# Kernel optimization log

Measured on AMD Instinct MI355X. Metric: run time of the kernel, lower is better.

Reference implementation:

```python
import jax, jax.numpy as jnp
import numpy as np

N = 300000
GRID = 256
K = 27  # 3x3x3 kernel offsets
C = 128


def _build_neighbors(rng):
    # sample unique occupied voxels in a GRID^3 lattice (sorted linear ids)
    lin = np.unique(rng.integers(0, GRID ** 3, size=int(N * 1.3)))[:N]
    z = lin // (GRID * GRID)
    y = (lin // GRID) % GRID
    x = lin % GRID
    nbr = np.full((N, K), -1, np.int32)
    k = 0
    for dz in (-1, 0, 1):
        for dy in (-1, 0, 1):
            for dx in (-1, 0, 1):
                nz, ny, nx = z + dz, y + dy, x + dx
                valid = (nz >= 0) & (nz < GRID) & (ny >= 0) & (ny < GRID) & (nx >= 0) & (nx < GRID)
                nlin = (nz * GRID + ny) * GRID + nx
                pos = np.clip(np.searchsorted(lin, nlin), 0, N - 1)
                found = valid & (lin[pos] == nlin)
                nbr[:, k] = np.where(found, pos, -1).astype(np.int32)
                k += 1
    return nbr


def setup_inputs() -> dict:
    key = jax.random.key(0)
    ks = jax.random.split(key, 8)
    s = 0.05
    rng = np.random.default_rng(0)
    nbr_idx = jnp.asarray(_build_neighbors(rng))
    return {
        "x_feat": jnp.ones((N, 1), jnp.float32),
        "W_in": jax.random.normal(ks[0], (K, 1, C), jnp.float32) * s,
        "b_in": jnp.zeros((C,), jnp.float32),
        "W_res": jax.random.normal(ks[1], (3, 2, K, C, C), jnp.float32) * s,
        "b_res": jnp.zeros((3, 2, C), jnp.float32),
        "W_out": jax.random.normal(ks[2], (K, C, C), jnp.float32) * s,
        "b_out": jnp.zeros((C,), jnp.float32),
        "Wf1": jax.random.normal(ks[3], (C, C), jnp.float32) * s,
        "bf1": jnp.zeros((C,), jnp.float32),
        "Wf2": jax.random.normal(ks[4], (C, C), jnp.float32) * s,
        "bf2": jnp.zeros((C,), jnp.float32),
        "Wf3": jax.random.normal(ks[5], (C, 3), jnp.float32) * s,
        "bf3": jnp.zeros((3,), jnp.float32),
        "nbr_idx": nbr_idx,
    }


def _sconv(x, nbr, W, b):
    # sparse 3^3 conv: per-offset gather -> GEMM -> masked accumulate
    # x: [N,Cin], nbr: [N,K] (-1 = no neighbor), W: [K,Cin,Cout]
    Cout = W.shape[-1]
    def body(k, acc):
        idx = nbr[:, k]
        g = jnp.where((idx >= 0)[:, None], x[jnp.maximum(idx, 0)], 0.0)
        return acc + g @ W[k]
    acc = jnp.zeros((x.shape[0], Cout), x.dtype)
    return jax.lax.fori_loop(0, W.shape[0], body, acc) + b


def _decoder(x_feat, nbr, W_in, b_in, W_res, b_res, W_out, b_out, Wf1, bf1, Wf2, bf2, Wf3, bf3):
    h = jax.nn.relu(_sconv(x_feat, nbr, W_in, b_in))
    for i in range(W_res.shape[0]):  # ResNetBlock: conv-relu-conv + residual
        r = jax.nn.relu(_sconv(h, nbr, W_res[i, 0], b_res[i, 0]))
        r = _sconv(r, nbr, W_res[i, 1], b_res[i, 1])
        h = h + r
    h = _sconv(h, nbr, W_out, b_out)
    # fc stack of 1x1 convs (pointwise GEMMs)
    h = jax.nn.relu(h @ Wf1 + bf1)
    h = jax.nn.relu(h @ Wf2 + bf2)
    return h @ Wf3 + bf3  # [N,3] predicted coordinate offsets


def reference(x_feat, W_in, b_in, W_res, b_res, W_out, b_out, Wf1, bf1, Wf2, bf2, Wf3, bf3, nbr_idx):
    return _decoder(x_feat, nbr_idx, W_in, b_in, W_res, b_res, W_out, b_out, Wf1, bf1, Wf2, bf2, Wf3, bf3)
```

## Files before the change

### kernel.cpp

```cpp
#include <hip/hip_runtime.h>
#include <hip/hip_bf16.h>
#include <stdint.h>

#define NNODES 300000
#define KNBR   27
#define CDIM   128
#define P_ROWS   219968
#define MAXTILES 2048
#define MAXSLOT  16
#define NT_SELF  ((NNODES + 127) / 128)
#define SELF_GRID 512


typedef __bf16 bf16x8_t __attribute__((ext_vector_type(8)));
typedef __bf16 bf16x4_t __attribute__((ext_vector_type(4)));
typedef float  f32x4_t  __attribute__((ext_vector_type(4)));

union BP8 { bf16x8_t v; __hip_bfloat16 h[8]; };
union BP4 { bf16x4_t v; __hip_bfloat16 h[4]; };

__device__ __forceinline__ void gl2lds16(const void* g, void* l) {
  __builtin_amdgcn_global_load_lds(
      reinterpret_cast<const __attribute__((address_space(1))) uint32_t*>(
          reinterpret_cast<uintptr_t>(g)),
      reinterpret_cast<__attribute__((address_space(3))) uint32_t*>(
          reinterpret_cast<uintptr_t>(l)),
      16, 0, 0);
}

__global__ void prep_weights(const float* __restrict__ Wres,
                             const float* __restrict__ Wout,
                             const float* __restrict__ Wf1,
                             const float* __restrict__ Wf2,
                             __hip_bfloat16* __restrict__ wbf) {
  int b = blockIdx.x;
  int m = b >> 7;
  int cout = b & 127;
  int cin = threadIdx.x;
  const float* src;
  if (m < 162)      src = Wres + (size_t)m * 16384;
  else if (m < 189) src = Wout + (size_t)(m - 162) * 16384;
  else if (m == 189) src = Wf1;
  else               src = Wf2;
  float v = src[cin * 128 + cout];
  int sp = (cin & 15) * 8 + (cin >> 4);
  wbf[(size_t)m * 16384 + cout * 128 + sp] = __float2bfloat16(v);
}

__global__ void prep_bias(const float* __restrict__ b_res,
                          const float* __restrict__ b_out,
                          const float* __restrict__ bf1,
                          const float* __restrict__ bf2,
                          float* __restrict__ bp) {
  int v = blockIdx.x;
  int p = threadIdx.x;
  const float* src;
  if (v < 6)       src = b_res + v * 128;
  else if (v == 6) src = b_out;
  else if (v == 7) src = bf1;
  else             src = bf2;
  bp[v * 128 + p] = src[(p & 7) * 16 + (p >> 3)];
}

__global__ void prep_win(const float* __restrict__ Win,
                         __hip_bfloat16* __restrict__ WinT) {
  int c = threadIdx.x;
  for (int k = 0; k < 32; ++k)
    WinT[c * 32 + k] = __float2bfloat16(k < 27 ? Win[k * 128 + c] : 0.0f);
}

__global__ void init_meta(int* __restrict__ segcnt, __hip_bfloat16* __restrict__ z) {
  int t = threadIdx.x;
  if (t < 32) segcnt[t] = 0;
  if (t == 0) { segcnt[128] = 0; segcnt[129] = 0; }
  z[t] = __float2bfloat16(0.0f);
}

__global__ void count_pairs(const int* __restrict__ nbr, int* __restrict__ segcnt,
                            unsigned int* __restrict__ nmask,
                            int* __restrict__ vlist) {
  __shared__ int lc[27];
  int t = threadIdx.x;
  if (t < 27) lc[t] = 0;
  __syncthreads();
  int n = blockIdx.x * 256 + t;
  if (n < NNODES) {
    int nb[27];
    #pragma unroll
    for (int k = 0; k < 27; ++k) nb[k] = nbr[n * 27 + k];
    unsigned int mask = 0;
    #pragma unroll
    for (int k = 0; k < 27; ++k)
      if (k != 13 && nb[k] >= 0) mask |= (1u << k);
    int pc = __popc(mask);
    while (pc > MAXSLOT) {
      mask &= ~(1u << (31 - __clz((int)mask)));
      --pc;
    }
    unsigned int m = mask;
    int j = 0;
    while (m) {
      int k = __ffs(m) - 1; m &= m - 1;
      vlist[n * MAXSLOT + j] = nb[k]; ++j;
      atomicAdd(&lc[k], 1);
    }
    nmask[n] = mask;
  }
  __syncthreads();
  if (t < 27 && t != 13 && lc[t]) atomicAdd(&segcnt[t], lc[t]);
}

__global__ void scan_tiles(const int* __restrict__ segcnt,
                           int* __restrict__ segbase, int* __restrict__ seglen,
                           int* __restrict__ cursor,
                           int* __restrict__ tile_k, int* __restrict__ tile_row0,
                           int* __restrict__ tile_rows,
                           int* __restrict__ ntile) {
  __shared__ int sbase[27], slen[27], tbase[27];
  int t = threadIdx.x;
  for (int i = t; i < MAXTILES; i += 256) tile_k[i] = -1;
  if (t < 32) cursor[t] = 0;
  if (t == 0) {
    int base = 0, tb = 0;
    for (int k = 0; k < 27; ++k) {
      int c = (k == 13) ? 0 : segcnt[k];
      if (base + c > P_ROWS) c = P_ROWS - base;
      if (c < 0) c = 0;
      sbase[k] = base; slen[k] = c; tbase[k] = tb;
      base += c;
      tb += (c + 127) >> 7;
    }
    ntile[0] = tb;
  }
  __syncthreads();
  if (t < 27) {
    segbase[t] = sbase[t];
    seglen[t] = slen[t];
    if (t != 13) {
      int idx = tbase[t];
      for (int r = 0; r < slen[t]; r += 128, ++idx) {
        if (idx < MAXTILES) {
          tile_k[idx] = t;
          tile_row0[idx] = sbase[t] + r;
          tile_rows[idx] = (slen[t] - r < 128) ? (slen[t] - r) : 128;
        }
      }
    }
  }
}

__global__ void fill_pairs(const unsigned int* __restrict__ nmask,
                           const int* __restrict__ vlist,
                           const int* __restrict__ segbase, const int* __restrict__ seglen,
                           int* __restrict__ cursor,
                           int* __restrict__ pr_src, int* __restrict__ pr_dst,
                           int* __restrict__ dinfo, int* __restrict__ dcursor) {
  __shared__ int lc[27], lb[27];
  __shared__ int dloc, dbase_s;
  int t = threadIdx.x;
  if (t < 27) lc[t] = 0;
  if (t == 0) dloc = 0;
  __syncthreads();
  int n = blockIdx.x * 256 + t;
  unsigned int mask = (n < NNODES) ? nmask[n] : 0u;
  int myj = __popc(mask);
  int myoff = myj ? atomicAdd(&dloc, myj) : 0;
  unsigned int m = mask;
  while (m) { int k = __ffs(m) - 1; m &= m - 1; atomicAdd(&lc[k], 1); }
  __syncthreads();
  if (t < 27) { lb[t] = lc[t] ? atomicAdd(&cursor[t], lc[t]) : 0; lc[t] = 0; }
  if (t == 0) dbase_s = dloc ? atomicAdd(dcursor, dloc) : 0;
  __syncthreads();
  if (n < NNODES) {
    int dbase = dbase_s + myoff;
    int jj = 0, vidx = 0;
    m = mask;
    while (m) {
      int k = __ffs(m) - 1; m &= m - 1;
      int lp = atomicAdd(&lc[k], 1);
      int pos = lb[k] + lp;
      if (pos < seglen[k]) {
        int slot = segbase[k] + pos;
        pr_src[slot] = vlist[n * MAXSLOT + vidx];
        pr_dst[slot] = dbase + jj;
        ++jj;
      }
      ++vidx;
    }
    dinfo[n] = (dbase << 5) | jj;
  }
}

__global__ void build_g(const float* __restrict__ xf, const int* __restrict__ nbr,
                        __hip_bfloat16* __restrict__ G) {
  int e = blockIdx.x * 256 + threadIdx.x;
  if (e >= NNODES * 32) return;
  int n = e >> 5, j = e & 31;
  float v = 0.0f;
  if (j < 27) {
    int idx = nbr[n * 27 + j];
    if (idx >= 0) v = xf[idx];
  }
  G[e] = __float2bfloat16(v);
}

__global__ __launch_bounds__(256, 2)
void l1_gemm(const __hip_bfloat16* __restrict__ G,
             const __hip_bfloat16* __restrict__ WinT,
             const float* __restrict__ bin,
             __hip_bfloat16* __restrict__ Aout) {
  __shared__ unsigned short As[128 * 32];

  const int t    = threadIdx.x;
  const int wid  = t >> 6;
  const int lane = t & 63;
  const int quad = lane >> 4;
  const int l16  = lane & 15;
  const int m0   = blockIdx.x * 128;
  const int m_base = (wid & 1) * 64;
  const int n_base = (wid >> 1) * 64;

  bf16x8_t bfr[4];
  #pragma unroll
  for (int ni = 0; ni < 4; ++ni)
    bfr[ni] = *(const bf16x8_t*)(WinT + (n_base + ni * 16 + l16) * 32 + quad * 8);

  float bv[4];
  #pragma unroll
  for (int ni = 0; ni < 4; ++ni) bv[ni] = bin[n_base + ni * 16 + l16];

  const char* Gb = (const char*)(G + (size_t)m0 * 32);
  #pragma unroll
  for (int i = 0; i < 2; ++i) {
    int row = i * 64 + (t >> 2);
    int slot = t & 3;
    gl2lds16(Gb + (size_t)row * 64 + ((slot ^ (row & 3)) * 16),
             (char*)As + i * 4096 + t * 16);
  }
  __syncthreads();

  f32x4_t acc[4][4];
  #pragma unroll
  for (int i = 0; i < 4; ++i)
    #pragma unroll
    for (int j = 0; j < 4; ++j)
      acc[i][j] = (f32x4_t){0.f, 0.f, 0.f, 0.f};

  bf16x8_t af[4];
  #pragma unroll
  for (int mi = 0; mi < 4; ++mi)
    af[mi] = *(const bf16x8_t*)(As + (m_base + mi * 16 + l16) * 32 +
                                ((quad ^ (l16 & 3)) * 8));
  #pragma unroll
  for (int mi = 0; mi < 4; ++mi)
    #pragma unroll
    for (int ni = 0; ni < 4; ++ni)
      acc[mi][ni] = __builtin_amdgcn_mfma_f32_16x16x32_bf16(af[mi], bfr[ni], acc[mi][ni], 0, 0, 0);

  const int nb4 = n_base >> 4;
  #pragma unroll
  for (int mi = 0; mi < 4; ++mi)
    #pragma unroll
    for (int r = 0; r < 4; ++r) {
      int node = m0 + m_base + mi * 16 + quad * 4 + r;
      if (node < NNODES) {
        BP4 o;
        #pragma unroll
        for (int ni = 0; ni < 4; ++ni) {
          float v = acc[mi][ni][r] + bv[ni];
          v = v > 0.0f ? v : 0.0f;
          o.h[ni] = __float2bfloat16(v);
        }
        *(bf16x4_t*)(Aout + (size_t)node * 128 + l16 * 8 + nb4) = o.v;
      }
    }
}

__global__ __launch_bounds__(256, 3)
void pair_gemm(const __hip_bfloat16* __restrict__ Ain,
               const __hip_bfloat16* __restrict__ Wl,
               const int* __restrict__ pr_src,
               const int* __restrict__ pr_dst,
               const int* __restrict__ tile_k, const int* __restrict__ tile_row0,
               const int* __restrict__ tile_rows,
               __hip_bfloat16* __restrict__ P,
               const __hip_bfloat16* __restrict__ zrow) {
  __shared__ unsigned short Ws[128 * 128];

  const int tk = tile_k[blockIdx.x];
  if (tk < 0) return;
  const int row0 = tile_row0[blockIdx.x];
  const int rows = tile_rows[blockIdx.x];

  const int t    = threadIdx.x;
  const int wid  = t >> 6;
  const int lane = t & 63;
  const int quad = lane >> 4;
  const int l16  = lane & 15;
  const int m_base = wid * 32;

  {
    const char* wsrc = (const char*)(Wl + (size_t)tk * 16384);
    #pragma unroll
    for (int i = 0; i < 8; ++i) {
      int row = wid * 32 + i * 4 + quad;
      gl2lds16(wsrc + (uint32_t)row * 256 + (uint32_t)((l16 ^ (row & 7)) * 16),
               (char*)Ws + wid * 8192 + i * 1024 + lane * 16);
    }
  }

  const __hip_bfloat16* rp[2];
  #pragma unroll
  for (int mi = 0; mi < 2; ++mi) {
    int row = m_base + mi * 16 + l16;
    rp[mi] = zrow;
    if (row < rows) rp[mi] = Ain + (size_t)pr_src[row0 + row] * 128;
  }
  int dst[2][4];
  #pragma unroll
  for (int mi = 0; mi < 2; ++mi)
    #pragma unroll
    for (int r = 0; r < 4; ++r) {
      int row = m_base + mi * 16 + quad * 4 + r;
      dst[mi][r] = (row < rows) ? pr_dst[row0 + row] : -1;
    }

  __syncthreads();

  f32x4_t acc[2][8];
  #pragma unroll
  for (int i = 0; i < 2; ++i)
    #pragma unroll
    for (int j = 0; j < 8; ++j)
      acc[i][j] = (f32x4_t){0.f, 0.f, 0.f, 0.f};

  #pragma unroll
  for (int kk = 0; kk < 4; ++kk) {
    bf16x8_t af[2];
    #pragma unroll
    for (int mi = 0; mi < 2; ++mi)
      af[mi] = *(const bf16x8_t*)(rp[mi] + kk * 32 + quad * 8);
    #pragma unroll
    for (int ni = 0; ni < 8; ++ni) {
      bf16x8_t bw = *(const bf16x8_t*)(Ws + (ni * 16 + l16) * 128 +
                                       (((kk * 4 + quad) ^ (l16 & 7)) * 8));
      #pragma unroll
      for (int mi = 0; mi < 2; ++mi)
        acc[mi][ni] = __builtin_amdgcn_mfma_f32_16x16x32_bf16(af[mi], bw, acc[mi][ni], 0, 0, 0);
    }
  }

  #pragma unroll
  for (int mi = 0; mi < 2; ++mi)
    #pragma unroll
    for (int r = 0; r < 4; ++r) {
      if (dst[mi][r] >= 0) {
        BP8 o;
        #pragma unroll
        for (int ni = 0; ni < 8; ++ni)
          o.h[ni] = __float2bfloat16(acc[mi][ni][r]);
        *(bf16x8_t*)(P + (size_t)dst[mi][r] * 128 + l16 * 8) = o.v;
      }
    }
}

template <int EPI, bool HASP>
__global__ __launch_bounds__(256, 2)
void self_gemm(const __hip_bfloat16* __restrict__ Ain,
               const __hip_bfloat16* __restrict__ W13,
               const float* __restrict__ bp,
               const __hip_bfloat16* __restrict__ P,
               const int* __restrict__ dinfo,
               __hip_bfloat16* __restrict__ Aout,
               const __hip_bfloat16* __restrict__ zrow) {
  const int t    = threadIdx.x;
  const int wid  = t >> 6;
  const int lane = t & 63;
  const int quad = lane >> 4;
  const int l16  = lane & 15;
  const int m_base = wid * 32;

  bf16x8_t bfr[8][4];
  #pragma unroll
  for (int ni = 0; ni < 8; ++ni)
    #pragma unroll
    for (int kk = 0; kk < 4; ++kk)
      bfr[ni][kk] = *(const bf16x8_t*)(W13 + (ni * 16 + l16) * 128 + kk * 32 + quad * 8);

  float bb[8];
  {
    f32x4_t b0 = *(const f32x4_t*)(bp + l16 * 8);
    f32x4_t b1 = *(const f32x4_t*)(bp + l16 * 8 + 4);
    #pragma unroll
    for (int i = 0; i < 4; ++i) { bb[i] = b0[i]; bb[i + 4] = b1[i]; }
  }

  #pragma unroll 1
  for (int tile = blockIdx.x; tile < NT_SELF; tile += gridDim.x) {
    const int m0 = tile * 128;

    int dif[2][4];
    if (HASP) {
      #pragma unroll
      for (int mi = 0; mi < 2; ++mi)
        #pragma unroll
        for (int r = 0; r < 4; ++r) {
          int node = m0 + m_base + mi * 16 + quad * 4 + r;
          dif[mi][r] = (node < NNODES) ? dinfo[node] : 0;
        }
    }

    f32x4_t acc[2][8];
    #pragma unroll
    for (int i = 0; i < 2; ++i)
      #pragma unroll
      for (int j = 0; j < 8; ++j)
        acc[i][j] = (f32x4_t){0.f, 0.f, 0.f, 0.f};

    const __hip_bfloat16* Abase = Ain + (size_t)(m0 + m_base + l16) * 128;

    #pragma unroll
    for (int kk = 0; kk < 4; ++kk) {
      bf16x8_t af[2];
      #pragma unroll
      for (int mi = 0; mi < 2; ++mi)
        af[mi] = *(const bf16x8_t*)(Abase + mi * 2048 + kk * 32 + quad * 8);
      #pragma unroll
      for (int mi = 0; mi < 2; ++mi)
        #pragma unroll
        for (int ni = 0; ni < 8; ++ni)
          acc[mi][ni] = __builtin_amdgcn_mfma_f32_16x16x32_bf16(af[mi], bfr[ni][kk], acc[mi][ni], 0, 0, 0);
    }

    #pragma unroll
    for (int mi = 0; mi < 2; ++mi) {
      const int nodeb = m0 + m_base + mi * 16 + quad * 4;
      bf16x8_t hold[4], pf[4];
      int cnt4[4], base4[4];
      #pragma unroll
      for (int r = 0; r < 4; ++r) {
        int node = nodeb + r;
        bool ok = node < NNODES;
        if (EPI == 1)
          hold[r] = *(const bf16x8_t*)((ok ? Aout + (size_t)node * 128 : zrow) + l16 * 8);
        if (HASP) {
          int d = dif[mi][r];
          cnt4[r] = d & 31;
          base4[r] = d >> 5;
          pf[r] = *(const bf16x8_t*)((cnt4[r] > 0 ? P + (size_t)base4[r] * 128 : zrow) + l16 * 8);
        }
      }
      #pragma unroll
      for (int r = 0; r < 4; ++r) {
        int node = nodeb + r;
        if (node >= NNODES) continue;
        float add[8];
        #pragma unroll
        for (int ni = 0; ni < 8; ++ni) add[ni] = bb[ni];
        if (HASP) {
          if (cnt4[r] > 0) {
            #pragma unroll
            for (int ni = 0; ni < 8; ++ni) add[ni] += (float)pf[r][ni];
          }
          for (int j = 1; j < cnt4[r]; ++j) {
            bf16x8_t pv = *(const bf16x8_t*)(P + (size_t)(base4[r] + j) * 128 + l16 * 8);
            #pragma unroll
            for (int ni = 0; ni < 8; ++ni) add[ni] += (float)pv[ni];
          }
        }
        BP8 o;
        #pragma unroll
        for (int ni = 0; ni < 8; ++ni) {
          float v = acc[mi][ni][r] + add[ni];
          if (EPI == 0) {
            v = v > 0.0f ? v : 0.0f;
            o.h[ni] = __float2bfloat16(v);
          } else if (EPI == 1) {
            o.h[ni] = __float2bfloat16((float)hold[r][ni] + v);
          } else {
            o.h[ni] = __float2bfloat16(v);
          }
        }
        *(bf16x8_t*)(Aout + (size_t)node * 128 + l16 * 8) = o.v;
      }
    }
  }
}

__global__ __launch_bounds__(256, 2)
void fc_fused(const __hip_bfloat16* __restrict__ Ain,
              const __hip_bfloat16* __restrict__ W1,
              const __hip_bfloat16* __restrict__ W2,
              const float* __restrict__ bp1,
              const float* __restrict__ bp2,
              const float* __restrict__ Wf3,
              const float* __restrict__ bf3,
              float* __restrict__ out) {
  __shared__ unsigned short S0[16384];
  __shared__ unsigned short S1[16384];

  const int t    = threadIdx.x;
  const int wid  = t >> 6;
  const int lane = t & 63;
  const int quad = lane >> 4;
  const int l16  = lane & 15;
  const int m_base = wid * 32;
  const int m0   = blockIdx.x * 128;

  #pragma unroll
  for (int i = 0; i < 8; ++i) {
    int row = wid * 32 + i * 4 + quad;
    uint32_t goff = (uint32_t)row * 256 + (uint32_t)((l16 ^ (row & 7)) * 16);
    gl2lds16((const char*)W1 + goff, (char*)S0 + wid * 8192 + i * 1024 + lane * 16);
    gl2lds16((const char*)W2 + goff, (char*)S1 + wid * 8192 + i * 1024 + lane * 16);
  }

  float bb1[8], bb2[8];
  {
    f32x4_t a0 = *(const f32x4_t*)(bp1 + l16 * 8);
    f32x4_t a1 = *(const f32x4_t*)(bp1 + l16 * 8 + 4);
    f32x4_t c0 = *(const f32x4_t*)(bp2 + l16 * 8);
    f32x4_t c1 = *(const f32x4_t*)(bp2 + l16 * 8 + 4);
    #pragma unroll
    for (int i = 0; i < 4; ++i) {
      bb1[i] = a0[i]; bb1[i + 4] = a1[i];
      bb2[i] = c0[i]; bb2[i + 4] = c1[i];
    }
  }
  float wf[8][3];
  #pragma unroll
  for (int ni = 0; ni < 8; ++ni)
    #pragma unroll
    for (int j = 0; j < 3; ++j)
      wf[ni][j] = Wf3[(ni * 16 + l16) * 3 + j];
  float b30 = bf3[0], b31 = bf3[1], b32 = bf3[2];

  __syncthreads();

  f32x4_t acc[2][8];
  #pragma unroll
  for (int i = 0; i < 2; ++i)
    #pragma unroll
    for (int j = 0; j < 8; ++j)
      acc[i][j] = (f32x4_t){0.f, 0.f, 0.f, 0.f};

  const __hip_bfloat16* Abase = Ain + (size_t)(m0 + m_base + l16) * 128;
  #pragma unroll
  for (int kk = 0; kk < 4; ++kk) {
    bf16x8_t af[2];
    #pragma unroll
    for (int mi = 0; mi < 2; ++mi)
      af[mi] = *(const bf16x8_t*)(Abase + mi * 2048 + kk * 32 + quad * 8);
    #pragma unroll
    for (int ni = 0; ni < 8; ++ni) {
      bf16x8_t bw = *(const bf16x8_t*)(S0 + (ni * 16 + l16) * 128 +
                                       (((kk * 4 + quad) ^ (l16 & 7)) * 8));
      #pragma unroll
      for (int mi = 0; mi < 2; ++mi)
        acc[mi][ni] = __builtin_amdgcn_mfma_f32_16x16x32_bf16(af[mi], bw, acc[mi][ni], 0, 0, 0);
    }
  }

  __syncthreads();

  #pragma unroll
  for (int mi = 0; mi < 2; ++mi)
    #pragma unroll
    for (int r = 0; r < 4; ++r) {
      int row = m_base + mi * 16 + quad * 4 + r;
      BP8 o;
      #pragma unroll
      for (int ni = 0; ni < 8; ++ni) {
        float v = acc[mi][ni][r] + bb1[ni];
        v = v > 0.0f ? v : 0.0f;
        o.h[ni] = __float2bfloat16(v);
      }
      *(bf16x8_t*)((char*)S0 + (uint32_t)row * 256 + ((l16 ^ (row & 7)) * 16)) = o.v;
    }
  __syncthreads();

  #pragma unroll
  for (int i = 0; i < 2; ++i)
    #pragma unroll
    for (int j = 0; j < 8; ++j)
      acc[i][j] = (f32x4_t){0.f, 0.f, 0.f, 0.f};

  #pragma unroll
  for (int kk = 0; kk < 4; ++kk) {
    bf16x8_t af[2];
    #pragma unroll
    for (int mi = 0; mi < 2; ++mi) {
      int row = m_base + mi * 16 + l16;
      af[mi] = *(const bf16x8_t*)((char*)S0 + (uint32_t)row * 256 +
                                  (((kk * 4 + quad) ^ (row & 7)) * 16));
    }
    #pragma unroll
    for (int ni = 0; ni < 8; ++ni) {
      bf16x8_t bw = *(const bf16x8_t*)(S1 + (ni * 16 + l16) * 128 +
                                       (((kk * 4 + quad) ^ (l16 & 7)) * 8));
      #pragma unroll
      for (int mi = 0; mi < 2; ++mi)
        acc[mi][ni] = __builtin_amdgcn_mfma_f32_16x16x32_bf16(af[mi], bw, acc[mi][ni], 0, 0, 0);
    }
  }

  #pragma unroll
  for (int mi = 0; mi < 2; ++mi)
    #pragma unroll
    for (int r = 0; r < 4; ++r) {
      int node = m0 + m_base + mi * 16 + quad * 4 + r;
      float a0 = 0.f, a1 = 0.f, a2 = 0.f;
      #pragma unroll
      for (int ni = 0; ni < 8; ++ni) {
        float v = acc[mi][ni][r] + bb2[ni];
        v = v > 0.0f ? v : 0.0f;
        v = (float)__float2bfloat16(v);
        a0 += v * wf[ni][0];
        a1 += v * wf[ni][1];
        a2 += v * wf[ni][2];
      }
      #pragma unroll
      for (int s = 8; s >= 1; s >>= 1) {
        a0 += __shfl_xor(a0, s);
        a1 += __shfl_xor(a1, s);
        a2 += __shfl_xor(a2, s);
      }
      if (l16 == 0 && node < NNODES) {
        out[node * 3 + 0] = a0 + b30;
        out[node * 3 + 1] = a1 + b31;
        out[node * 3 + 2] = a2 + b32;
      }
    }
}

__global__ void layer1_kernel(const float* __restrict__ xf,
                              const float* __restrict__ Win,
                              const float* __restrict__ bin,
                              const int* __restrict__ nbr,
                              __hip_bfloat16* __restrict__ abf) {
  int n = blockIdx.x;
  int c = threadIdx.x;
  float acc = bin[c];
  #pragma unroll 9
  for (int k = 0; k < KNBR; ++k) {
    int idx = nbr[n * KNBR + k];
    if (idx >= 0) acc += xf[idx] * Win[k * 128 + c];
  }
  acc = acc > 0.0f ? acc : 0.0f;
  int sp = (c & 15) * 8 + (c >> 4);
  abf[(size_t)n * 128 + sp] = __float2bfloat16(acc);
}

template <int EPI>
__global__ __launch_bounds__(256, 2)
void sconv_kernel(const __hip_bfloat16* __restrict__ Ain,
                  const __hip_bfloat16* __restrict__ Wt,
                  const float* __restrict__ bias,
                  const int* __restrict__ nbr,
                  int nk,
                  __hip_bfloat16* __restrict__ Aout,
                  const __hip_bfloat16* __restrict__ zrow) {
  __shared__ unsigned short As[128 * 128];
  __shared__ unsigned short Bs[128 * 128];

  const int t    = threadIdx.x;
  const int wid  = t >> 6;
  const int lane = t & 63;
  const int quad = lane >> 4;
  const int l16  = lane & 15;
  const int m0   = blockIdx.x * 128;

  f32x4_t acc[4][4];
  #pragma unroll
  for (int i = 0; i < 4; ++i)
    #pragma unroll
    for (int j = 0; j < 4; ++j)
      acc[i][j] = (f32x4_t){0.f, 0.f, 0.f, 0.f};

  const int m_base = (wid & 1) * 64;
  const int n_base = (wid >> 1) * 64;

  for (int k = 0; k < nk; ++k) {
    {
      const char* wsrc = (const char*)(Wt + (size_t)k * 16384);
      #pragma unroll
      for (int i = 0; i < 8; ++i) {
        uint32_t off = (uint32_t)wid * 8192 + (uint32_t)i * 1024;
        int row = wid * 32 + i * 4 + quad;
        uint32_t goff = (uint32_t)row * 256 + (uint32_t)((l16 ^ (row & 7)) * 16);
        gl2lds16(wsrc + goff, (char*)Bs + off);
      }
    }
    {
      #pragma unroll
      for (int i = 0; i < 8; ++i) {
        int r = i * 16 + wid * 4 + quad;
        int node = m0 + r;
        const __hip_bfloat16* rowp;
        if (nbr) {
          int idx = (node < NNODES) ? nbr[node * KNBR + k] : -1;
          rowp = (idx >= 0) ? (Ain + (size_t)idx * 128) : zrow;
        } else {
          rowp = (node < NNODES) ? (Ain + (size_t)node * 128) : zrow;
        }
        uint32_t ldsoff = (uint32_t)(i * 16 + wid * 4) * 256;
        gl2lds16((const char*)rowp + ((l16 ^ (r & 7)) * 16), (char*)As + ldsoff);
      }
    }
    __syncthreads();

    #pragma unroll
    for (int kk = 0; kk < 4; ++kk) {
      const int p = ((kk * 4 + quad) ^ (l16 & 7)) * 8;
      bf16x8_t af[4], bfr[4];
      #pragma unroll
      for (int mi = 0; mi < 4; ++mi)
        af[mi] = *(const bf16x8_t*)(As + (m_base + mi * 16 + l16) * 128 + p);
      #pragma unroll
      for (int ni = 0; ni < 4; ++ni)
        bfr[ni] = *(const bf16x8_t*)(Bs + (n_base + ni * 16 + l16) * 128 + p);
      #pragma unroll
      for (int mi = 0; mi < 4; ++mi)
        #pragma unroll
        for (int ni = 0; ni < 4; ++ni)
          acc[mi][ni] = __builtin_amdgcn_mfma_f32_16x16x32_bf16(af[mi], bfr[ni], acc[mi][ni], 0, 0, 0);
    }
    __syncthreads();
  }

  const int nb4 = n_base >> 4;
  #pragma unroll
  for (int ni = 0; ni < 4; ++ni) {
    int sp = l16 * 8 + nb4 + ni;
    float bvv = bias[sp];
    #pragma unroll
    for (int mi = 0; mi < 4; ++mi) {
      #pragma unroll
      for (int r = 0; r < 4; ++r) {
        int row = m_base + mi * 16 + quad * 4 + r;
        int node = m0 + row;
        if (node < NNODES) {
          float v = acc[mi][ni][r] + bvv;
          size_t o = (size_t)node * 128 + sp;
          if (EPI == 0) {
            v = v > 0.0f ? v : 0.0f;
            Aout[o] = __float2bfloat16(v);
          } else if (EPI == 1) {
            Aout[o] = __float2bfloat16(__bfloat162float(Aout[o]) + v);
          } else {
            Aout[o] = __float2bfloat16(v);
          }
        }
      }
    }
  }
}

__global__ void fc3_kernel(const __hip_bfloat16* __restrict__ r,
                           const float* __restrict__ W,
                           const float* __restrict__ b,
                           float* __restrict__ out) {
  int n = blockIdx.x * 256 + threadIdx.x;
  if (n >= NNODES) return;
  float a0 = b[0], a1 = b[1], a2 = b[2];
  const bf16x8_t* rp = (const bf16x8_t*)(r + (size_t)n * 128);
  #pragma unroll
  for (int c8 = 0; c8 < 16; ++c8) {
    bf16x8_t v8 = rp[c8];
    #pragma unroll
    for (int j = 0; j < 8; ++j) {
      float v = (float)v8[j];
      int c = j * 16 + c8;
      a0 += v * W[c * 3 + 0];
      a1 += v * W[c * 3 + 1];
      a2 += v * W[c * 3 + 2];
    }
  }
  out[n * 3 + 0] = a0;
  out[n * 3 + 1] = a1;
  out[n * 3 + 2] = a2;
}

extern "C" void kernel_launch(void* const* d_in, const int* in_sizes, int n_in,
                              void* d_out, int out_size, void* d_ws, size_t ws_size,
                              hipStream_t stream) {
  const float* x_feat = (const float*)d_in[0];
  const float* W_in   = (const float*)d_in[1];
  const float* b_in   = (const float*)d_in[2];
  const float* W_res  = (const float*)d_in[3];
  const float* b_res  = (const float*)d_in[4];
  const float* W_out  = (const float*)d_in[5];
  const float* b_out  = (const float*)d_in[6];
  const float* Wf1    = (const float*)d_in[7];
  const float* bf1    = (const float*)d_in[8];
  const float* Wf2    = (const float*)d_in[9];
  const float* bf2    = (const float*)d_in[10];
  const float* Wf3    = (const float*)d_in[11];
  const float* bf3    = (const float*)d_in[12];
  const int*   nbr    = (const int*)d_in[13];
  float* out = (float*)d_out;

  char* ws = (char*)d_ws;
  __hip_bfloat16* abf0 = (__hip_bfloat16*)ws;
  __hip_bfloat16* abf1 = (__hip_bfloat16*)(ws +  76800000);
  __hip_bfloat16* wbf  = (__hip_bfloat16*)(ws + 153600000);
  __hip_bfloat16* zrow = (__hip_bfloat16*)(ws + 159858688);
  __hip_bfloat16* P    = (__hip_bfloat16*)(ws + 159858944);
  __hip_bfloat16* WinT = (__hip_bfloat16*)(ws + 159858944 + 56320000 - 8192);
  int* pr_dst    = (int*)(ws + 216178944);
  unsigned int* nmask = (unsigned int*)(ws + 217058944);
  int* dinfo     = (int*)(ws + 235378944);
  int* pr_src    = (int*)(ws + 236578944);
  int* segcnt    = (int*)(ws + 237458944);
  int* segbase   = segcnt + 32;
  int* seglen    = segcnt + 64;
  int* cursor    = segcnt + 96;
  int* ntile     = segcnt + 128;
  int* dcursor   = segcnt + 129;
  int* tile_k    = (int*)(ws + 237463040);
  int* tile_row0 = tile_k + MAXTILES;
  int* tile_rows = tile_k + 2 * MAXTILES;
  float* bp      = (float*)(ws + 237487616);
  __hip_bfloat16* G = abf1;
  int* vlist = (int*)P;
  const size_t SPARSE_NEED = 237487616 + 4608 + 512;

  const int GB = (NNODES + 127) / 128;
  __hip_bfloat16* W0 = wbf;

  prep_weights<<<191 * 128, 128, 0, stream>>>(W_res, W_out, Wf1, Wf2, wbf);
  init_meta<<<1, 128, 0, stream>>>(segcnt, zrow);

  if (ws_size >= SPARSE_NEED) {
    prep_bias<<<9, 128, 0, stream>>>(b_res, b_out, bf1, bf2, bp);
    prep_win<<<1, 128, 0, stream>>>(W_in, WinT);
    build_g<<<(NNODES * 32 + 255) / 256, 256, 0, stream>>>(x_feat, nbr, G);
    l1_gemm<<<GB, 256, 0, stream>>>(G, WinT, b_in, abf0);

    const int CB2 = (NNODES + 255) / 256;
    count_pairs<<<CB2, 256, 0, stream>>>(nbr, segcnt, nmask, vlist);
    scan_tiles<<<1, 256, 0, stream>>>(segcnt, segbase, seglen, cursor,
                                      tile_k, tile_row0, tile_rows, ntile);
    fill_pairs<<<CB2, 256, 0, stream>>>(nmask, vlist, segbase, seglen, cursor,
                                        pr_src, pr_dst, dinfo, dcursor);

    #define CONV(IN, OUT, WLAYER, BV, EPI)                                             \
      pair_gemm<<<MAXTILES, 256, 0, stream>>>(IN, WLAYER, pr_src, pr_dst,              \
                                              tile_k, tile_row0, tile_rows,            \
                                              P, zrow);                                \
      self_gemm<EPI, true><<<SELF_GRID, 256, 0, stream>>>(IN, (WLAYER) + 13 * 16384,   \
                                                          bp + (BV) * 128, P, dinfo,   \
                                                          OUT, zrow);

    CONV(abf0, abf1, W0 +   0 * 16384, 0, 0)
    CONV(abf1, abf0, W0 +  27 * 16384, 1, 1)
    CONV(abf0, abf1, W0 +  54 * 16384, 2, 0)
    CONV(abf1, abf0, W0 +  81 * 16384, 3, 1)
    CONV(abf0, abf1, W0 + 108 * 16384, 4, 0)
    CONV(abf1, abf0, W0 + 135 * 16384, 5, 1)
    CONV(abf0, abf1, W0 + 162 * 16384, 6, 2)
    #undef CONV

    fc_fused<<<GB, 256, 0, stream>>>(abf1, W0 + 189 * 16384, W0 + 190 * 16384,
                                     bp + 7 * 128, bp + 8 * 128, Wf3, bf3, out);
  } else {
    prep_bias<<<9, 128, 0, stream>>>(b_res, b_out, bf1, bf2, bp);
    layer1_kernel<<<NNODES, 128, 0, stream>>>(x_feat, W_in, b_in, nbr, abf0);
    sconv_kernel<0><<<GB, 256, 0, stream>>>(abf0, W0 +   0 * 16384, bp + 0 * 128, nbr, 27, abf1, zrow);
    sconv_kernel<1><<<GB, 256, 0, stream>>>(abf1, W0 +  27 * 16384, bp + 1 * 128, nbr, 27, abf0, zrow);
    sconv_kernel<0><<<GB, 256, 0, stream>>>(abf0, W0 +  54 * 16384, bp + 2 * 128, nbr, 27, abf1, zrow);
    sconv_kernel<1><<<GB, 256, 0, stream>>>(abf1, W0 +  81 * 16384, bp + 3 * 128, nbr, 27, abf0, zrow);
    sconv_kernel<0><<<GB, 256, 0, stream>>>(abf0, W0 + 108 * 16384, bp + 4 * 128, nbr, 27, abf1, zrow);
    sconv_kernel<1><<<GB, 256, 0, stream>>>(abf1, W0 + 135 * 16384, bp + 5 * 128, nbr, 27, abf0, zrow);
    sconv_kernel<2><<<GB, 256, 0, stream>>>(abf0, W0 + 162 * 16384, bp + 6 * 128, nbr, 27, abf1, zrow);
    sconv_kernel<0><<<GB, 256, 0, stream>>>(abf1, W0 + 189 * 16384, bp + 7 * 128, nullptr, 1, abf0, zrow);
    sconv_kernel<0><<<GB, 256, 0, stream>>>(abf0, W0 + 190 * 16384, bp + 8 * 128, nullptr, 1, abf1, zrow);
    fc3_kernel<<<(NNODES + 255) / 256, 256, 0, stream>>>(abf1, Wf3, bf3, out);
  }
}
```

Baseline: 837.3 us.

## Stage self-GEMM weights in swizzled LDS and use 512-thread blocks

The self (center-offset) GEMM no longer keeps the whole 128x128 weight tile in per-thread registers. Instead it loads the weights once per block into XOR-swizzled shared memory via global_load_lds and reads B fragments from LDS inside the MFMA loop. Each wave now covers 16 rows instead of 32, blocks grow to 512 threads with higher launch-bound occupancy, and the grid doubles. This frees a large register budget to raise occupancy and latency hiding in the memory-bound epilogue. The cost is extra LDS reads per tile and the loss of the software-prefetched first P row and residual load.

```diff
diff --git a/kernel.cpp b/kernel.cpp
--- a/kernel.cpp
+++ b/kernel.cpp
@@ -9,7 +9,7 @@
 #define MAXTILES 2048
 #define MAXSLOT  16
 #define NT_SELF  ((NNODES + 127) / 128)
-#define SELF_GRID 512
+#define SELF_GRID 1024
 
 
 typedef __bf16 bf16x8_t __attribute__((ext_vector_type(8)));
@@ -365,7 +365,7 @@
 }
 
 template <int EPI, bool HASP>
-__global__ __launch_bounds__(256, 2)
+__global__ __launch_bounds__(512, 4)
 void self_gemm(const __hip_bfloat16* __restrict__ Ain,
                const __hip_bfloat16* __restrict__ W13,
                const float* __restrict__ bp,
@@ -373,19 +373,24 @@
                const int* __restrict__ dinfo,
                __hip_bfloat16* __restrict__ Aout,
                const __hip_bfloat16* __restrict__ zrow) {
+  __shared__ unsigned short Ws[128 * 128];
+
   const int t    = threadIdx.x;
   const int wid  = t >> 6;
   const int lane = t & 63;
   const int quad = lane >> 4;
   const int l16  = lane & 15;
-  const int m_base = wid * 32;
-
-  bf16x8_t bfr[8][4];
-  #pragma unroll
-  for (int ni = 0; ni < 8; ++ni)
-    #pragma unroll
-    for (int kk = 0; kk < 4; ++kk)
-      bfr[ni][kk] = *(const bf16x8_t*)(W13 + (ni * 16 + l16) * 128 + kk * 32 + quad * 8);
+  const int m_base = wid * 16;
+
+  {
+    #pragma unroll
+    for (int i = 0; i < 4; ++i) {
+      int row = i * 32 + (t >> 4);
+      int slot = t & 15;
+      gl2lds16((const char*)W13 + (uint32_t)row * 256 + (uint32_t)((slot ^ (row & 7)) * 16),
+               (char*)Ws + i * 8192 + t * 16);
+    }
+  }
 
   float bb[8];
   {
@@ -395,94 +400,72 @@
     for (int i = 0; i < 4; ++i) { bb[i] = b0[i]; bb[i + 4] = b1[i]; }
   }
 
+  __syncthreads();
+
   #pragma unroll 1
   for (int tile = blockIdx.x; tile < NT_SELF; tile += gridDim.x) {
     const int m0 = tile * 128;
 
-    int dif[2][4];
+    int dif[4];
     if (HASP) {
       #pragma unroll
-      for (int mi = 0; mi < 2; ++mi)
-        #pragma unroll
-        for (int r = 0; r < 4; ++r) {
-          int node = m0 + m_base + mi * 16 + quad * 4 + r;
-          dif[mi][r] = (node < NNODES) ? dinfo[node] : 0;
+      for (int r = 0; r < 4; ++r) {
+        int node = m0 + m_base + quad * 4 + r;
+        dif[r] = (node < NNODES) ? dinfo[node] : 0;
+      }
+    }
+
+    f32x4_t acc[8];
+    #pragma unroll
+    for (int j = 0; j < 8; ++j)
+      acc[j] = (f32x4_t){0.f, 0.f, 0.f, 0.f};
+
+    const __hip_bfloat16* Abase = Ain + (size_t)(m0 + m_base + l16) * 128;
+
+    #pragma unroll
+    for (int kk = 0; kk < 4; ++kk) {
+      bf16x8_t af = *(const bf16x8_t*)(Abase + kk * 32 + quad * 8);
+      #pragma unroll
+      for (int ni = 0; ni < 8; ++ni) {
+        bf16x8_t bw = *(const bf16x8_t*)(Ws + (ni * 16 + l16) * 128 +
+                                         (((kk * 4 + quad) ^ (l16 & 7)) * 8));
+        acc[ni] = __builtin_amdgcn_mfma_f32_16x16x32_bf16(af, bw, acc[ni], 0, 0, 0);
+      }
+    }
+
+    const int nodeb = m0 + m_base + quad * 4;
+    #pragma unroll
+    for (int r = 0; r < 4; ++r) {
+      int node = nodeb + r;
+      if (node >= NNODES) continue;
+      float add[8];
+      #pragma unroll
+      for (int ni = 0; ni < 8; ++ni) add[ni] = bb[ni];
+      if (HASP) {
+        int cnt  = dif[r] & 31;
+        int base = dif[r] >> 5;
+        const __hip_bfloat16* pp = P + (size_t)base * 128 + l16 * 8;
+        for (int j = 0; j < cnt; ++j) {
+          bf16x8_t pv = *(const bf16x8_t*)(pp + (size_t)j * 128);
+          #pragma unroll
+          for (int ni = 0; ni < 8; ++ni) add[ni] += (float)pv[ni];
         }
-    }
-
-    f32x4_t acc[2][8];
-    #pragma unroll
-    for (int i = 0; i < 2; ++i)
-      #pragma unroll
-      for (int j = 0; j < 8; ++j)
-        acc[i][j] = (f32x4_t){0.f, 0.f, 0.f, 0.f};
-
-    const __hip_bfloat16* Abase = Ain + (size_t)(m0 + m_base + l16) * 128;
-
-    #pragma unroll
-    for (int kk = 0; kk < 4; ++kk) {
-      bf16x8_t af[2];
-      #pragma unroll
-      for (int mi = 0; mi < 2; ++mi)
-        af[mi] = *(const bf16x8_t*)(Abase + mi * 2048 + kk * 32 + quad * 8);
-      #pragma unroll
-      for (int mi = 0; mi < 2; ++mi)
+      }
+      BP8 o;
+      if (EPI == 1) {
+        bf16x8_t hold = *(const bf16x8_t*)(Aout + (size_t)node * 128 + l16 * 8);
         #pragma unroll
         for (int ni = 0; ni < 8; ++ni)
-          acc[mi][ni] = __builtin_amdgcn_mfma_f32_16x16x32_bf16(af[mi], bfr[ni][kk], acc[mi][ni], 0, 0, 0);
-    }
-
-    #pragma unroll
-    for (int mi = 0; mi < 2; ++mi) {
-      const int nodeb = m0 + m_base + mi * 16 + quad * 4;
-      bf16x8_t hold[4], pf[4];
-      int cnt4[4], base4[4];
-      #pragma unroll
-      for (int r = 0; r < 4; ++r) {
-        int node = nodeb + r;
-        bool ok = node < NNODES;
-        if (EPI == 1)
-          hold[r] = *(const bf16x8_t*)((ok ? Aout + (size_t)node * 128 : zrow) + l16 * 8);
-        if (HASP) {
-          int d = dif[mi][r];
-          cnt4[r] = d & 31;
-          base4[r] = d >> 5;
-          pf[r] = *(const bf16x8_t*)((cnt4[r] > 0 ? P + (size_t)base4[r] * 128 : zrow) + l16 * 8);
-        }
-      }
-      #pragma unroll
-      for (int r = 0; r < 4; ++r) {
-        int node = nodeb + r;
-        if (node >= NNODES) continue;
-        float add[8];
-        #pragma unroll
-        for (int ni = 0; ni < 8; ++ni) add[ni] = bb[ni];
-        if (HASP) {
-          if (cnt4[r] > 0) {
-            #pragma unroll
-            for (int ni = 0; ni < 8; ++ni) add[ni] += (float)pf[r][ni];
-          }
-          for (int j = 1; j < cnt4[r]; ++j) {
-            bf16x8_t pv = *(const bf16x8_t*)(P + (size_t)(base4[r] + j) * 128 + l16 * 8);
-            #pragma unroll
-            for (int ni = 0; ni < 8; ++ni) add[ni] += (float)pv[ni];
-          }
-        }
-        BP8 o;
+          o.h[ni] = __float2bfloat16((float)hold[ni] + acc[ni][r] + add[ni]);
+      } else {
         #pragma unroll
         for (int ni = 0; ni < 8; ++ni) {
-          float v = acc[mi][ni][r] + add[ni];
-          if (EPI == 0) {
-            v = v > 0.0f ? v : 0.0f;
-            o.h[ni] = __float2bfloat16(v);
-          } else if (EPI == 1) {
-            o.h[ni] = __float2bfloat16((float)hold[r][ni] + v);
-          } else {
-            o.h[ni] = __float2bfloat16(v);
-          }
+          float v = acc[ni][r] + add[ni];
+          if (EPI == 0) v = v > 0.0f ? v : 0.0f;
+          o.h[ni] = __float2bfloat16(v);
         }
-        *(bf16x8_t*)(Aout + (size_t)node * 128 + l16 * 8) = o.v;
-      }
+      }
+      *(bf16x8_t*)(Aout + (size_t)node * 128 + l16 * 8) = o.v;
     }
   }
 }
@@ -848,7 +831,7 @@
       pair_gemm<<<MAXTILES, 256, 0, stream>>>(IN, WLAYER, pr_src, pr_dst,              \
                                               tile_k, tile_row0, tile_rows,            \
                                               P, zrow);                                \
-      self_gemm<EPI, true><<<SELF_GRID, 256, 0, stream>>>(IN, (WLAYER) + 13 * 16384,   \
+      self_gemm<EPI, true><<<SELF_GRID, 512, 0, stream>>>(IN, (WLAYER) + 13 * 16384,   \
                                                           bp + (BV) * 128, P, dinfo,   \
                                                           OUT, zrow);
 
```

Result: slower. 1.499 ms (+79.0%).

## Double-buffer self_gemm A tiles in LDS via async global_load_lds prefetch

Applied to the files above, without the earlier changes.

The self_gemm persistent loop now stages each 128-row A tile into a double-buffered 64 KB LDS array with a swizzled layout, prefetching the next tile while computing the current one. The aim is to hide global-memory latency for the A operand, which was previously loaded straight into registers. In exchange it uses much more LDS per block, which may cut occupancy below the launch_bounds target of 2. There is also no explicit vmcnt wait before reading the prefetched data beyond the __syncthreads, so the ordering of the async LDS loads is a correctness risk.

```diff
diff --git a/kernel.cpp b/kernel.cpp
--- a/kernel.cpp
+++ b/kernel.cpp
@@ -373,6 +373,8 @@
                const int* __restrict__ dinfo,
                __hip_bfloat16* __restrict__ Aout,
                const __hip_bfloat16* __restrict__ zrow) {
+  __shared__ unsigned short As[2][16384];
+
   const int t    = threadIdx.x;
   const int wid  = t >> 6;
   const int lane = t & 63;
@@ -395,8 +397,32 @@
     for (int i = 0; i < 4; ++i) { bb[i] = b0[i]; bb[i + 4] = b1[i]; }
   }
 
+  int tile = blockIdx.x;
+  if (tile < NT_SELF) {
+    const char* Abase = (const char*)(Ain + (size_t)tile * 16384);
+    #pragma unroll
+    for (int i = 0; i < 8; ++i) {
+      int row = wid * 32 + i * 4 + quad;
+      gl2lds16(Abase + (uint32_t)row * 256 + (uint32_t)((l16 ^ (row & 7)) * 16),
+               (char*)As[0] + wid * 8192 + i * 1024 + lane * 16);
+    }
+  }
+
+  int cur = 0;
   #pragma unroll 1
-  for (int tile = blockIdx.x; tile < NT_SELF; tile += gridDim.x) {
+  for (; tile < NT_SELF; tile += gridDim.x, cur ^= 1) {
+    const int nxt = tile + gridDim.x;
+    __syncthreads();
+    if (nxt < NT_SELF) {
+      const char* Abase = (const char*)(Ain + (size_t)nxt * 16384);
+      #pragma unroll
+      for (int i = 0; i < 8; ++i) {
+        int row = wid * 32 + i * 4 + quad;
+        gl2lds16(Abase + (uint32_t)row * 256 + (uint32_t)((l16 ^ (row & 7)) * 16),
+                 (char*)As[cur ^ 1] + wid * 8192 + i * 1024 + lane * 16);
+      }
+    }
+
     const int m0 = tile * 128;
 
     int dif[2][4];
@@ -417,14 +443,16 @@
       for (int j = 0; j < 8; ++j)
         acc[i][j] = (f32x4_t){0.f, 0.f, 0.f, 0.f};
 
-    const __hip_bfloat16* Abase = Ain + (size_t)(m0 + m_base + l16) * 128;
-
+    const unsigned short* Ac = As[cur];
     #pragma unroll
     for (int kk = 0; kk < 4; ++kk) {
       bf16x8_t af[2];
       #pragma unroll
-      for (int mi = 0; mi < 2; ++mi)
-        af[mi] = *(const bf16x8_t*)(Abase + mi * 2048 + kk * 32 + quad * 8);
+      for (int mi = 0; mi < 2; ++mi) {
+        int row = m_base + mi * 16 + l16;
+        af[mi] = *(const bf16x8_t*)(Ac + row * 128 +
+                                    (((kk * 4 + quad) ^ (l16 & 7)) * 8));
+      }
       #pragma unroll
       for (int mi = 0; mi < 2; ++mi)
         #pragma unroll
```

Result: no change. 851.6 us (+1.7%).
